# Kernel tuning notes

Measured on AMD Instinct MI355X. Metric: run time of the kernel, lower is better.

The kernel has to match this reference:

```python
import jax, jax.numpy as jnp
import numpy as np

EMBED_DIM = 768
NUM_HEADS = 12
HEAD_DIM = EMBED_DIM // NUM_HEADS  # 64
SCALE = HEAD_DIM ** 0.5  # NOTE: source MULTIPLIES by sqrt(head_dim) (likely a bug, kept faithful)


def setup_inputs() -> dict:
    key = jax.random.key(0)
    kx, kq, kk, kv, ko = jax.random.split(key, 5)
    B, N, E = 8, 2048, EMBED_DIM
    s = 1.0 / np.sqrt(E)
    return {
        "x": jax.random.normal(kx, (B, N, E), dtype=jnp.float32),
        # nn.Linear weights stored [out_features, in_features], y = x @ W.T
        "Wq": jax.random.normal(kq, (E, E), dtype=jnp.float32) * s,
        "Wk": jax.random.normal(kk, (E, E), dtype=jnp.float32) * s,
        "Wv": jax.random.normal(kv, (E, E), dtype=jnp.float32) * s,
        "Wo": jax.random.normal(ko, (E, E), dtype=jnp.float32) * s,
    }


def reference(x, Wq, Wk, Wv, Wo):
    # Projections (no bias)
    q = jnp.einsum("bne,fe->bnf", x, Wq)
    k = jnp.einsum("bne,fe->bnf", x, Wk)
    v = jnp.einsum("bne,fe->bnf", x, Wv)
    # Full-width attention over the entire embedding dim (no head split, per source)
    energy = jnp.einsum("bid,bjd->bij", q, k) * SCALE  # [B, N, N]
    attn = jax.nn.softmax(energy, axis=-1)
    out = jnp.einsum("bij,bjd->bid", attn, v)  # [B, N, E]
    return jnp.einsum("bne,fe->bnf", out, Wo)
```

## Files before the change

### kernel.cpp

```cpp
#include <hip/hip_runtime.h>
#include <stdint.h>

typedef __bf16 bf16;
typedef __bf16 bf16x4 __attribute__((ext_vector_type(4)));
typedef __bf16 bf16x8 __attribute__((ext_vector_type(8)));
typedef float  f32x4  __attribute__((ext_vector_type(4)));

constexpr int BB = 8;
constexpr int NN = 2048;
constexpr int EE = 768;
constexpr int MM = BB * NN;
constexpr int E2 = 2 * EE;

typedef const __attribute__((address_space(1))) void* as1_cvp;
typedef __attribute__((address_space(3))) void* as3_vp;

static __device__ __forceinline__ void gld16(const void* g, void* l) {
  __builtin_amdgcn_global_load_lds((as1_cvp)g, (as3_vp)l, 16, 0, 0);
}

__global__ __launch_bounds__(256) void k_splitx(const float4* __restrict__ x,
                                                bf16x4* __restrict__ hi,
                                                bf16x4* __restrict__ lo, int n4) {
  int i = blockIdx.x * 256 + threadIdx.x;
  int st = gridDim.x * 256;
  for (; i < n4; i += st) {
    float4 v = x[i];
    bf16x4 h, l;
    h[0] = (bf16)v.x; l[0] = (bf16)(v.x - (float)h[0]);
    h[1] = (bf16)v.y; l[1] = (bf16)(v.y - (float)h[1]);
    h[2] = (bf16)v.z; l[2] = (bf16)(v.z - (float)h[2]);
    h[3] = (bf16)v.w; l[3] = (bf16)(v.w - (float)h[3]);
    hi[i] = h; lo[i] = l;
  }
}

__global__ __launch_bounds__(256) void k_wprep(const float4* __restrict__ wq,
                                               const float4* __restrict__ wk,
                                               const float4* __restrict__ wo,
                                               bf16x4* __restrict__ qkh, bf16x4* __restrict__ qkl,
                                               bf16x4* __restrict__ ob) {
  const int n4 = EE * EE / 4;
  int sel = blockIdx.y;
  int i = blockIdx.x * 256 + threadIdx.x;
  int st = gridDim.x * 256;
  for (; i < n4; i += st) {
    if (sel <= 1) {
      float4 v = sel == 0 ? wq[i] : wk[i];
      bf16x4 h, l;
      h[0] = (bf16)v.x; l[0] = (bf16)(v.x - (float)h[0]);
      h[1] = (bf16)v.y; l[1] = (bf16)(v.y - (float)h[1]);
      h[2] = (bf16)v.z; l[2] = (bf16)(v.z - (float)h[2]);
      h[3] = (bf16)v.w; l[3] = (bf16)(v.w - (float)h[3]);
      int o = i + sel * n4;
      qkh[o] = h; qkl[o] = l;
    } else {
      float4 v = wo[i];
      bf16x4 h;
      h[0] = (bf16)v.x; h[1] = (bf16)v.y; h[2] = (bf16)v.z; h[3] = (bf16)v.w;
      ob[i] = h;
    }
  }
}

__global__ __launch_bounds__(256) void k_wtrans(const float* __restrict__ src,
                                                bf16* __restrict__ dst) {
  __shared__ float t[64][65];
  int e0 = blockIdx.x * 64, f0 = blockIdx.y * 64;
  int tid = threadIdx.x;
#pragma unroll
  for (int h = 0; h < 4; h++) {
    int lin = h * 1024 + tid * 4;
    int r = lin >> 6, c = lin & 63;
    float4 v = *(const float4*)(src + (size_t)(f0 + r) * EE + e0 + c);
    t[r][c] = v.x; t[r][c + 1] = v.y; t[r][c + 2] = v.z; t[r][c + 3] = v.w;
  }
  __syncthreads();
#pragma unroll
  for (int h = 0; h < 4; h++) {
    int lin = h * 1024 + tid * 4;
    int er = lin >> 6, fc = lin & 63;
    bf16x4 o;
#pragma unroll
    for (int j = 0; j < 4; j++) o[j] = (bf16)t[fc + j][er];
    *(bf16x4*)(dst + (size_t)(e0 + er) * EE + f0 + fc) = o;
  }
}

template <bool SPLIT, int EPI>
__global__ __launch_bounds__(256, 2) void k_gemm(
    const bf16* __restrict__ Ah, const bf16* __restrict__ Al,
    const bf16* __restrict__ Bh, const bf16* __restrict__ Bl,
    void* __restrict__ C0, void* __restrict__ C1,
    int Kdim, int lda, int ldb, int ldc,
    long long sA, long long sB, long long sC, float cscale) {
  constexpr int NTILES = SPLIT ? 4 : 2;
  __shared__ __align__(16) bf16 smm[NTILES * 128 * 64];
  bf16* smAh = smm;
  bf16* smBh = smm + 128 * 64;
  bf16* smAl = SPLIT ? smm + 2 * 128 * 64 : nullptr;
  bf16* smBl = SPLIT ? smm + 3 * 128 * 64 : nullptr;

  const int tid = threadIdx.x;
  const int lane = tid & 63, wid = tid >> 6;
  const int lr = lane & 15, lq = lane >> 4;
  const int wr = (wid >> 1) * 64, wc = (wid & 1) * 64;
  const long long bz = blockIdx.z;
  const int col0 = blockIdx.x * 128, row0 = blockIdx.y * 128;

  const bf16* pAh = Ah + bz * sA;
  const bf16* pBh = Bh + bz * sB;
  const bf16* pAl = SPLIT ? (Al + bz * sA) : nullptr;
  const bf16* pBl = SPLIT ? (Bl + bz * sB) : nullptr;

  f32x4 acc[4][4] = {};

  for (int kt = 0; kt < Kdim; kt += 64) {
    {
      int o = tid * 16;
#pragma unroll
      for (int r = 0; r < 4; r++, o += 4096) {
        int row = o >> 7;
        int c = (o & 127) ^ ((row & 7) << 4);
        gld16((const char*)(pAh + (size_t)(row0 + row) * lda + kt) + c, (char*)smAh + o);
        gld16((const char*)(pBh + (size_t)(col0 + row) * ldb + kt) + c, (char*)smBh + o);
        if constexpr (SPLIT) {
          gld16((const char*)(pAl + (size_t)(row0 + row) * lda + kt) + c, (char*)smAl + o);
          gld16((const char*)(pBl + (size_t)(col0 + row) * ldb + kt) + c, (char*)smBl + o);
        }
      }
    }
    __syncthreads();
#pragma unroll
    for (int kk = 0; kk < 2; kk++) {
      bf16x8 ah[4], bh[4], al[4], bl[4];
#pragma unroll
      for (int i = 0; i < 4; i++) {
        int ar = wr + i * 16 + lr;
        int ao = ar * 128 + ((kk * 64 + lq * 16) ^ ((ar & 7) << 4));
        ah[i] = *(const bf16x8*)((const char*)smAh + ao);
        int br = wc + i * 16 + lr;
        int bo = br * 128 + ((kk * 64 + lq * 16) ^ ((br & 7) << 4));
        bh[i] = *(const bf16x8*)((const char*)smBh + bo);
        if constexpr (SPLIT) {
          al[i] = *(const bf16x8*)((const char*)smAl + ao);
          bl[i] = *(const bf16x8*)((const char*)smBl + bo);
        }
      }
#pragma unroll
      for (int i = 0; i < 4; i++)
#pragma unroll
        for (int j = 0; j < 4; j++) {
          acc[i][j] = __builtin_amdgcn_mfma_f32_16x16x32_bf16(ah[i], bh[j], acc[i][j], 0, 0, 0);
          if constexpr (SPLIT) {
            acc[i][j] = __builtin_amdgcn_mfma_f32_16x16x32_bf16(ah[i], bl[j], acc[i][j], 0, 0, 0);
            acc[i][j] = __builtin_amdgcn_mfma_f32_16x16x32_bf16(al[i], bh[j], acc[i][j], 0, 0, 0);
          }
        }
    }
    __syncthreads();
  }

#pragma unroll
  for (int i = 0; i < 4; i++) {
#pragma unroll
    for (int j2 = 0; j2 < 4; j2++) {
      f32x4 v = acc[i][j2];
#pragma unroll
      for (int j = 0; j < 4; j++) {
        size_t r = (size_t)(row0 + wr + i * 16 + lq * 4 + j);
        size_t c = (size_t)(col0 + wc + j2 * 16 + lr);
        size_t idx = r * (size_t)ldc + c;
        float val = v[j] * cscale;
        if constexpr (EPI == 0) {
          bf16* Chp = (bf16*)C0 + bz * sC;
          bf16* Clp = (bf16*)C1 + bz * sC;
          bf16 h = (bf16)val;
          Chp[idx] = h;
          Clp[idx] = (bf16)(val - (float)h);
        } else if constexpr (EPI == 1) {
          float* Cp = (float*)C0 + bz * sC;
          Cp[idx] = val;
        } else {
          bf16* Cp = (bf16*)C0 + bz * sC;
          Cp[idx] = (bf16)val;
        }
      }
    }
  }
}

__global__ __launch_bounds__(256) void k_softmax(float* __restrict__ S) {
  size_t row = blockIdx.x;
  float* srow = S + row * (size_t)NN;
  int tid = threadIdx.x;
  int wid = tid >> 6, lane = tid & 63;
  const float4* s4 = (const float4*)srow;
  float4 v0 = s4[tid * 2], v1 = s4[tid * 2 + 1];
  float vv[8] = {v0.x, v0.y, v0.z, v0.w, v1.x, v1.y, v1.z, v1.w};
  float m = vv[0];
#pragma unroll
  for (int j = 1; j < 8; j++) m = fmaxf(m, vv[j]);
#pragma unroll
  for (int d = 1; d < 64; d <<= 1) m = fmaxf(m, __shfl_xor(m, d));
  __shared__ float red[8];
  if (lane == 0) red[wid] = m;
  __syncthreads();
  m = fmaxf(fmaxf(red[0], red[1]), fmaxf(red[2], red[3]));
  float e[8];
  float ssum = 0.f;
#pragma unroll
  for (int j = 0; j < 8; j++) { e[j] = __expf(vv[j] - m); ssum += e[j]; }
#pragma unroll
  for (int d = 1; d < 64; d <<= 1) ssum += __shfl_xor(ssum, d);
  if (lane == 0) red[4 + wid] = ssum;
  __syncthreads();
  ssum = red[4] + red[5] + red[6] + red[7];
  float inv = 1.0f / ssum;
  bf16x8 p;
#pragma unroll
  for (int j = 0; j < 8; j++) p[j] = (bf16)(e[j] * inv);
  *(bf16x8*)((bf16*)srow + tid * 8) = p;
}

extern "C" void kernel_launch(void* const* d_in, const int* in_sizes, int n_in,
                              void* d_out, int out_size, void* d_ws, size_t ws_size,
                              hipStream_t stream) {
  const float* x  = (const float*)d_in[0];
  const float* Wq = (const float*)d_in[1];
  const float* Wk = (const float*)d_in[2];
  const float* Wv = (const float*)d_in[3];
  const float* Wo = (const float*)d_in[4];
  float* out = (float*)d_out;
  char* ws = (char*)d_ws;

  const size_t szXE = (size_t)MM * EE * 2;
  const size_t szWb = (size_t)EE * EE * 2;
  const size_t szQKh = (size_t)MM * E2 * 2;
  const size_t szS1 = (size_t)NN * NN * 4;

  bf16* xhi = (bf16*)(ws);
  bf16* xlo = (bf16*)(ws + szXE);
  char* wb  = ws + 2 * szXE;
  bf16* wqkh = (bf16*)(wb);
  bf16* wqkl = (bf16*)(wb + 2 * szWb);
  bf16* wvT  = (bf16*)(wb + 4 * szWb);
  bf16* wob  = (bf16*)(wb + 5 * szWb);
  bf16* wvob = (bf16*)(wb + 6 * szWb);
  char* qkb = wb + 7 * szWb;
  bf16* QKh = (bf16*)(qkb);
  bf16* QKl = (bf16*)(qkb + szQKh);
  bf16* Ut  = (bf16*)(qkb + 2 * szQKh);
  char* Sb  = qkb + 2 * szQKh + szXE;
  float* S  = (float*)Sb;

  size_t oS = (size_t)(Sb - ws);
  size_t avail = ws_size > oS ? ws_size - oS : 0;
  int G = 8;
  while (G > 1 && (size_t)G * szS1 > avail) G >>= 1;

  k_splitx<<<2048, 256, 0, stream>>>((const float4*)x, (bf16x4*)xhi, (bf16x4*)xlo, MM * EE / 4);
  k_wprep<<<dim3(144, 3), 256, 0, stream>>>((const float4*)Wq, (const float4*)Wk,
                                            (const float4*)Wo,
                                            (bf16x4*)wqkh, (bf16x4*)wqkl, (bf16x4*)wob);
  k_wtrans<<<dim3(12, 12), 256, 0, stream>>>(Wv, wvT);

  k_gemm<true, 0><<<dim3(E2 / 128, MM / 128, 1), 256, 0, stream>>>(
      xhi, xlo, wqkh, wqkl, QKh, QKl, EE, EE, EE, E2, 0, 0, 0, 1.0f);
  k_gemm<false, 2><<<dim3(EE / 128, EE / 128, 1), 256, 0, stream>>>(
      wob, nullptr, wvT, nullptr, wvob, nullptr, EE, EE, EE, EE, 0, 0, 0, 1.0f);
  k_gemm<false, 2><<<dim3(MM / 128, EE / 128, 1), 256, 0, stream>>>(
      wvob, nullptr, xhi, nullptr, Ut, nullptr, EE, EE, EE, MM, 0, 0, 0, 1.0f);

  const long long sQK = (long long)NN * E2;
  for (int g = 0; g < BB; g += G) {
    const bf16* Qh = QKh + (size_t)g * NN * E2;
    const bf16* Ql = QKl + (size_t)g * NN * E2;
    k_gemm<true, 1><<<dim3(NN / 128, NN / 128, G), 256, 0, stream>>>(
        Qh, Ql, Qh + EE, Ql + EE, S, nullptr, EE, E2, E2, NN,
        sQK, sQK, (long long)NN * NN, 8.0f);
    k_softmax<<<G * NN, 256, 0, stream>>>(S);
    k_gemm<false, 1><<<dim3(EE / 128, NN / 128, G), 256, 0, stream>>>(
        (const bf16*)S, nullptr, Ut + (size_t)g * NN, nullptr,
        out + (size_t)g * NN * EE, nullptr, NN, 2 * NN, MM, EE,
        2LL * NN * NN, (long long)NN, (long long)NN * EE, 1.0f);
  }
}
```

Measured before the change: 435.3 us.

## Fold Wq and Wk into one combined weight so energy uses x directly

Rather than projecting x into separate Q and K and then forming Q·K^T, this precomputes Wq^T·Wk as one 768x768 weight (kept as a split bf16 pair), projects x once into Y, and computes energy as Y·x^T. The projection GEMM shrinks from 2E to E output columns, and the Q/K intermediate buffer goes away. The non-split GEMMs also get a higher launch-bounds occupancy hint. The cost is an extra small weight GEMM, plus a different rounding path through the combined weight that may change accuracy.

```diff
diff --git a/kernel.cpp b/kernel.cpp
--- a/kernel.cpp
+++ b/kernel.cpp
@@ -10,7 +10,6 @@
 constexpr int NN = 2048;
 constexpr int EE = 768;
 constexpr int MM = BB * NN;
-constexpr int E2 = 2 * EE;
 
 typedef const __attribute__((address_space(1))) void* as1_cvp;
 typedef __attribute__((address_space(3))) void* as3_vp;
@@ -35,36 +34,22 @@
   }
 }
 
-__global__ __launch_bounds__(256) void k_wprep(const float4* __restrict__ wq,
-                                               const float4* __restrict__ wk,
-                                               const float4* __restrict__ wo,
-                                               bf16x4* __restrict__ qkh, bf16x4* __restrict__ qkl,
-                                               bf16x4* __restrict__ ob) {
-  const int n4 = EE * EE / 4;
-  int sel = blockIdx.y;
+__global__ __launch_bounds__(256) void k_cvt(const float4* __restrict__ src,
+                                             bf16x4* __restrict__ dst, int n4) {
   int i = blockIdx.x * 256 + threadIdx.x;
   int st = gridDim.x * 256;
   for (; i < n4; i += st) {
-    if (sel <= 1) {
-      float4 v = sel == 0 ? wq[i] : wk[i];
-      bf16x4 h, l;
-      h[0] = (bf16)v.x; l[0] = (bf16)(v.x - (float)h[0]);
-      h[1] = (bf16)v.y; l[1] = (bf16)(v.y - (float)h[1]);
-      h[2] = (bf16)v.z; l[2] = (bf16)(v.z - (float)h[2]);
-      h[3] = (bf16)v.w; l[3] = (bf16)(v.w - (float)h[3]);
-      int o = i + sel * n4;
-      qkh[o] = h; qkl[o] = l;
-    } else {
-      float4 v = wo[i];
-      bf16x4 h;
-      h[0] = (bf16)v.x; h[1] = (bf16)v.y; h[2] = (bf16)v.z; h[3] = (bf16)v.w;
-      ob[i] = h;
-    }
-  }
-}
-
+    float4 v = src[i];
+    bf16x4 h;
+    h[0] = (bf16)v.x; h[1] = (bf16)v.y; h[2] = (bf16)v.z; h[3] = (bf16)v.w;
+    dst[i] = h;
+  }
+}
+
+template <bool PAIR>
 __global__ __launch_bounds__(256) void k_wtrans(const float* __restrict__ src,
-                                                bf16* __restrict__ dst) {
+                                                bf16* __restrict__ hi,
+                                                bf16* __restrict__ lo) {
   __shared__ float t[64][65];
   int e0 = blockIdx.x * 64, f0 = blockIdx.y * 64;
   int tid = threadIdx.x;
@@ -80,15 +65,21 @@
   for (int h = 0; h < 4; h++) {
     int lin = h * 1024 + tid * 4;
     int er = lin >> 6, fc = lin & 63;
-    bf16x4 o;
-#pragma unroll
-    for (int j = 0; j < 4; j++) o[j] = (bf16)t[fc + j][er];
-    *(bf16x4*)(dst + (size_t)(e0 + er) * EE + f0 + fc) = o;
-  }
-}
-
-template <bool SPLIT, int EPI>
-__global__ __launch_bounds__(256, 2) void k_gemm(
+    bf16x4 oh, ol;
+#pragma unroll
+    for (int j = 0; j < 4; j++) {
+      float v = t[fc + j][er];
+      bf16 hh = (bf16)v;
+      oh[j] = hh;
+      if constexpr (PAIR) ol[j] = (bf16)(v - (float)hh);
+    }
+    *(bf16x4*)(hi + (size_t)(e0 + er) * EE + f0 + fc) = oh;
+    if constexpr (PAIR) *(bf16x4*)(lo + (size_t)(e0 + er) * EE + f0 + fc) = ol;
+  }
+}
+
+template <bool SPLIT, int EPI, int LB>
+__global__ __launch_bounds__(256, LB) void k_gemm(
     const bf16* __restrict__ Ah, const bf16* __restrict__ Al,
     const bf16* __restrict__ Bh, const bf16* __restrict__ Bl,
     void* __restrict__ C0, void* __restrict__ C1,
@@ -236,23 +227,26 @@
 
   const size_t szXE = (size_t)MM * EE * 2;
   const size_t szWb = (size_t)EE * EE * 2;
-  const size_t szQKh = (size_t)MM * E2 * 2;
   const size_t szS1 = (size_t)NN * NN * 4;
 
   bf16* xhi = (bf16*)(ws);
   bf16* xlo = (bf16*)(ws + szXE);
   char* wb  = ws + 2 * szXE;
-  bf16* wqkh = (bf16*)(wb);
-  bf16* wqkl = (bf16*)(wb + 2 * szWb);
+  bf16* wqTh = (bf16*)(wb);
+  bf16* wqTl = (bf16*)(wb + 1 * szWb);
+  bf16* wkTh = (bf16*)(wb + 2 * szWb);
+  bf16* wkTl = (bf16*)(wb + 3 * szWb);
   bf16* wvT  = (bf16*)(wb + 4 * szWb);
   bf16* wob  = (bf16*)(wb + 5 * szWb);
-  bf16* wvob = (bf16*)(wb + 6 * szWb);
-  char* qkb = wb + 7 * szWb;
-  bf16* QKh = (bf16*)(qkb);
-  bf16* QKl = (bf16*)(qkb + szQKh);
-  bf16* Ut  = (bf16*)(qkb + 2 * szQKh);
-  char* Sb  = qkb + 2 * szQKh + szXE;
-  float* S  = (float*)Sb;
+  bf16* wqkTh = (bf16*)(wb + 6 * szWb);
+  bf16* wqkTl = (bf16*)(wb + 7 * szWb);
+  bf16* wvob  = (bf16*)(wb + 8 * szWb);
+  char* yb = wb + 9 * szWb;
+  bf16* Yh = (bf16*)(yb);
+  bf16* Yl = (bf16*)(yb + szXE);
+  bf16* Ut = (bf16*)(yb + 2 * szXE);
+  char* Sb = yb + 3 * szXE;
+  float* S = (float*)Sb;
 
   size_t oS = (size_t)(Sb - ws);
   size_t avail = ws_size > oS ? ws_size - oS : 0;
@@ -260,27 +254,28 @@
   while (G > 1 && (size_t)G * szS1 > avail) G >>= 1;
 
   k_splitx<<<2048, 256, 0, stream>>>((const float4*)x, (bf16x4*)xhi, (bf16x4*)xlo, MM * EE / 4);
-  k_wprep<<<dim3(144, 3), 256, 0, stream>>>((const float4*)Wq, (const float4*)Wk,
-                                            (const float4*)Wo,
-                                            (bf16x4*)wqkh, (bf16x4*)wqkl, (bf16x4*)wob);
-  k_wtrans<<<dim3(12, 12), 256, 0, stream>>>(Wv, wvT);
-
-  k_gemm<true, 0><<<dim3(E2 / 128, MM / 128, 1), 256, 0, stream>>>(
-      xhi, xlo, wqkh, wqkl, QKh, QKl, EE, EE, EE, E2, 0, 0, 0, 1.0f);
-  k_gemm<false, 2><<<dim3(EE / 128, EE / 128, 1), 256, 0, stream>>>(
+  k_cvt<<<64, 256, 0, stream>>>((const float4*)Wo, (bf16x4*)wob, EE * EE / 4);
+  k_wtrans<true><<<dim3(12, 12), 256, 0, stream>>>(Wq, wqTh, wqTl);
+  k_wtrans<true><<<dim3(12, 12), 256, 0, stream>>>(Wk, wkTh, wkTl);
+  k_wtrans<false><<<dim3(12, 12), 256, 0, stream>>>(Wv, wvT, nullptr);
+
+  k_gemm<true, 0, 2><<<dim3(EE / 128, EE / 128, 1), 256, 0, stream>>>(
+      wkTh, wkTl, wqTh, wqTl, wqkTh, wqkTl, EE, EE, EE, EE, 0, 0, 0, 1.0f);
+  k_gemm<false, 2, 4><<<dim3(EE / 128, EE / 128, 1), 256, 0, stream>>>(
       wob, nullptr, wvT, nullptr, wvob, nullptr, EE, EE, EE, EE, 0, 0, 0, 1.0f);
-  k_gemm<false, 2><<<dim3(MM / 128, EE / 128, 1), 256, 0, stream>>>(
+  k_gemm<true, 0, 2><<<dim3(EE / 128, MM / 128, 1), 256, 0, stream>>>(
+      xhi, xlo, wqkTh, wqkTl, Yh, Yl, EE, EE, EE, EE, 0, 0, 0, 1.0f);
+  k_gemm<false, 2, 4><<<dim3(MM / 128, EE / 128, 1), 256, 0, stream>>>(
       wvob, nullptr, xhi, nullptr, Ut, nullptr, EE, EE, EE, MM, 0, 0, 0, 1.0f);
 
-  const long long sQK = (long long)NN * E2;
+  const long long sNE = (long long)NN * EE;
   for (int g = 0; g < BB; g += G) {
-    const bf16* Qh = QKh + (size_t)g * NN * E2;
-    const bf16* Ql = QKl + (size_t)g * NN * E2;
-    k_gemm<true, 1><<<dim3(NN / 128, NN / 128, G), 256, 0, stream>>>(
-        Qh, Ql, Qh + EE, Ql + EE, S, nullptr, EE, E2, E2, NN,
-        sQK, sQK, (long long)NN * NN, 8.0f);
+    k_gemm<true, 1, 2><<<dim3(NN / 128, NN / 128, G), 256, 0, stream>>>(
+        Yh + (size_t)g * sNE, Yl + (size_t)g * sNE,
+        xhi + (size_t)g * sNE, xlo + (size_t)g * sNE,
+        S, nullptr, EE, EE, EE, NN, sNE, sNE, (long long)NN * NN, 8.0f);
     k_softmax<<<G * NN, 256, 0, stream>>>(S);
-    k_gemm<false, 1><<<dim3(EE / 128, NN / 128, G), 256, 0, stream>>>(
+    k_gemm<false, 1, 4><<<dim3(EE / 128, NN / 128, G), 256, 0, stream>>>(
         (const bf16*)S, nullptr, Ut + (size_t)g * NN, nullptr,
         out + (size_t)g * NN * EE, nullptr, NN, 2 * NN, MM, EE,
         2LL * NN * NN, (long long)NN, (long long)NN * EE, 1.0f);
```

New measurement: 418.9 us (median of 3 runs). 3.8% less time.
